# Performance work log

Measured on AMD Instinct MI355X. Metric: run time of the kernel, lower is better.

Reference implementation:

```python
import jax, jax.numpy as jnp
import numpy as np

NEG = 1e12  # matches torch code's -1e12 masking constant


def _rope_sincos(seq_len, dim, dtype):
    # SinusoidalPositionEmbedding with merge_mode='zero':
    # emb[n, i] pairs -> reshape to [n, dim] as [sin0, cos0, sin1, cos1, ...]
    pos = jnp.arange(seq_len, dtype=jnp.float32)
    inv = jnp.power(10000.0, -2.0 * jnp.arange(dim // 2, dtype=jnp.float32) / dim)
    ang = pos[:, None] * inv[None, :]            # [n, d/2]
    sin, cos = jnp.sin(ang), jnp.cos(ang)
    # cos_pos = pos[..., 1::2].repeat_interleave(2) == repeat(cos, 2)
    cos_pos = jnp.repeat(cos, 2, axis=-1).astype(dtype)  # [n, d]
    sin_pos = jnp.repeat(sin, 2, axis=-1).astype(dtype)  # [n, d]
    return sin_pos, cos_pos


def _rotate_half(x):
    # stack([-x[..., 1::2], x[..., ::2]], -1).reshape(x.shape)
    x2 = jnp.stack([-x[..., 1::2], x[..., ::2]], axis=-1)
    return x2.reshape(x.shape)


def setup_inputs() -> dict:
    key = jax.random.key(0)
    k1, k2, k3 = jax.random.split(key, 3)
    B, N, H = 8, 1024, 768
    heads, head_size = 12, 64
    inputs = jax.random.normal(k1, (B, N, H), dtype=jnp.float32)
    mask = jnp.ones((B, N), dtype=jnp.float32)
    W = jax.random.normal(k2, (H, heads * head_size * 2), dtype=jnp.float32) * (H ** -0.5)
    b = jnp.zeros((heads * head_size * 2,), dtype=jnp.float32)
    return {"inputs": inputs, "mask": mask, "W": W, "b": b}


def reference(inputs, mask, W, b):
    heads, head_size = 12, 64
    B, N, _ = inputs.shape
    x = inputs @ W + b                              # [B, N, heads*head_size*2]
    x = x.reshape(B, N, heads, 2 * head_size)       # split+stack over heads
    qw, kw = x[..., :head_size], x[..., head_size:]  # [B, N, heads, d]

    sin_pos, cos_pos = _rope_sincos(N, head_size, inputs.dtype)
    sin_pos = sin_pos[None, :, None, :]             # [1, N, 1, d]
    cos_pos = cos_pos[None, :, None, :]
    qw = qw * cos_pos + _rotate_half(qw) * sin_pos
    kw = kw * cos_pos + _rotate_half(kw) * sin_pos

    logits = jnp.einsum('bmhd,bnhd->bhmn', qw, kw)  # [B, heads, N, N]

    m1 = mask[:, None, :, None]                     # mask rows (axis ndim-2)
    m2 = mask[:, None, None, :]                     # mask cols (axis ndim-1)
    logits = logits * m1 + (-NEG) * (1.0 - m1)
    logits = logits * m2 + (-NEG) * (1.0 - m2)
    tril = jnp.tril(jnp.ones((N, N), dtype=logits.dtype), k=-1)
    logits = logits - tril * NEG                    # forbid end < start
    return logits / (head_size ** 0.5)
```

## Files before the change

kernel.cpp:

```cpp
#include <hip/hip_runtime.h>
#include <stdint.h>

#define NEGC 1000000000000.0f

using f32x4  = __attribute__((ext_vector_type(4))) float;
using short8 = __attribute__((ext_vector_type(8))) short;

typedef __attribute__((address_space(3))) uint32_t* lds_ptr_t;
typedef const __attribute__((address_space(1))) uint32_t* gptr_t;

__device__ __forceinline__ void gload_lds16(const void* g, const void* l) {
  __builtin_amdgcn_global_load_lds((gptr_t)g, (lds_ptr_t)l, 16, 0, 0);
}

__device__ __forceinline__ unsigned short f2bf(float f) {
  union { float f; uint32_t u; } v; v.f = f;
  uint32_t u = v.u;
  return (unsigned short)((u + 0x7fffu + ((u >> 16) & 1u)) >> 16);
}

__global__ __launch_bounds__(256) void k_prep(
    const float* __restrict__ in, unsigned short* __restrict__ inb,
    const float* __restrict__ W, unsigned short* __restrict__ Wt,
    float* __restrict__ ssin, float* __restrict__ scos) {
  __shared__ float tile[64][65];
  const int bx = blockIdx.x, t = threadIdx.x;
  if (bx < 6144) {
    int idx = bx * 256 + t;
    float4 v = ((const float4*)in)[idx];
    ushort4 o;
    o.x = f2bf(v.x); o.y = f2bf(v.y); o.z = f2bf(v.z); o.w = f2bf(v.w);
    ((ushort4*)inb)[idx] = o;
  } else if (bx < 6432) {
    int b = bx - 6144;
    int kb = b % 12, nb = b / 12;
    int c = t & 63, r0 = t >> 6;
#pragma unroll
    for (int p = 0; p < 16; ++p) {
      int r = r0 + p * 4;
      tile[r][c] = W[(size_t)(kb * 64 + r) * 1536 + nb * 64 + c];
    }
    __syncthreads();
#pragma unroll
    for (int p = 0; p < 16; ++p) {
      int n = r0 + p * 4;
      Wt[(size_t)(nb * 64 + n) * 768 + kb * 64 + c] = f2bf(tile[c][n]);
    }
  } else {
    int idx = (bx - 6432) * 256 + t;
    int m = idx >> 5, i = idx & 31;
    float inv = expf(-(float)i * (9.210340371976184f / 32.0f));
    float ang = (float)m * inv;
    ssin[idx] = sinf(ang);
    scos[idx] = cosf(ang);
  }
}

__global__ __launch_bounds__(256) void k_gemm1(
    const unsigned short* __restrict__ A,
    const unsigned short* __restrict__ Bt,
    const float* __restrict__ bias,
    const float* __restrict__ ssin, const float* __restrict__ scos,
    unsigned short* __restrict__ qb, unsigned short* __restrict__ kb) {
  __shared__ __align__(16) unsigned short As[2][128 * 64];
  __shared__ __align__(16) unsigned short Bs[2][128 * 64];
  const int tid = threadIdx.x;
  const int wave = tid >> 6, lane = tid & 63;
  const int wm = wave >> 1, wn = wave & 1;
  const int orig = blockIdx.x;
  const int xcd = orig & 7, idx = orig >> 3;
  const int mt8 = idx / 12;
  const int h   = idx - mt8 * 12;
  const int m0  = (xcd * 8 + mt8) * 128;
  const int j0  = h * 128;
  const int lr = lane >> 3, kc = lane & 7;

  f32x4 acc[4][4] = {};

#define STAGE1(buf, kt)                                                              \
  {                                                                                  \
    const int k0_ = (kt) * 64;                                                       \
    _Pragma("unroll")                                                                \
    for (int i = 0; i < 4; ++i) {                                                    \
      int row = i * 32 + wave * 8 + lr;                                              \
      int gk = k0_ + ((kc ^ (row & 7)) << 3);                                        \
      gload_lds16(&A[(size_t)(m0 + row) * 768 + gk], &As[buf][(i * 32 + wave * 8) * 64]); \
    }                                                                                \
    _Pragma("unroll")                                                                \
    for (int i = 0; i < 4; ++i) {                                                    \
      int row = i * 32 + wave * 8 + lr;                                              \
      int gk = k0_ + ((kc ^ (row & 7)) << 3);                                        \
      gload_lds16(&Bt[(size_t)(j0 + row) * 768 + gk], &Bs[buf][(i * 32 + wave * 8) * 64]); \
    }                                                                                \
  }

  STAGE1(0, 0);
  asm volatile("s_waitcnt vmcnt(0)" ::: "memory");
  __syncthreads();

  int cur = 0;
  for (int kt = 0; kt < 12; ++kt) {
    if (kt < 11) STAGE1(cur ^ 1, kt + 1);
#pragma unroll
    for (int kh = 0; kh < 2; ++kh) {
      short8 af[4], bfr[4];
#pragma unroll
      for (int mt = 0; mt < 4; ++mt) {
        int row = wm * 64 + mt * 16 + (lane & 15);
        int cs = (kh * 4 + (lane >> 4)) ^ (row & 7);
        af[mt] = *(const short8*)&As[cur][row * 64 + cs * 8];
      }
#pragma unroll
      for (int nt = 0; nt < 4; ++nt) {
        int row = wn * 64 + nt * 16 + (lane & 15);
        int cs = (kh * 4 + (lane >> 4)) ^ (row & 7);
        bfr[nt] = *(const short8*)&Bs[cur][row * 64 + cs * 8];
      }
#pragma unroll
      for (int mt = 0; mt < 4; ++mt)
#pragma unroll
        for (int nt = 0; nt < 4; ++nt)
          acc[mt][nt] = __builtin_amdgcn_mfma_f32_16x16x32_bf16(af[mt], bfr[nt], acc[mt][nt], 0, 0, 0);
    }
    if (kt < 11) {
      asm volatile("s_waitcnt vmcnt(0)" ::: "memory");
      __syncthreads();
      cur ^= 1;
    }
  }
#undef STAGE1

  const int col = lane & 15, rquad = lane >> 4;
  unsigned short* dst = (wn == 0) ? qb : kb;
#pragma unroll
  for (int nt = 0; nt < 4; ++nt) {
    const int d = nt * 16 + col;
    const float bv = bias[j0 + wn * 64 + d];
    const int ifr = d >> 1;
    const float sgn = (d & 1) ? 1.0f : -1.0f;
#pragma unroll
    for (int mt = 0; mt < 4; ++mt) {
#pragma unroll
      for (int j = 0; j < 4; ++j) {
        int mg = m0 + wm * 64 + mt * 16 + rquad * 4 + j;
        int ms = mg & 1023, bi = mg >> 10;
        float v = acc[mt][nt][j] + bv;
        float p = __shfl_xor(v, 1, 64);
        float s = ssin[ms * 32 + ifr], cv = scos[ms * 32 + ifr];
        float r = v * cv + sgn * p * s;
        dst[(size_t)((bi * 12 + h) * 1024 + ms) * 64 + d] = f2bf(r);
      }
    }
  }
}

__global__ __launch_bounds__(256) void k_gemm2(
    const unsigned short* __restrict__ qb, const unsigned short* __restrict__ kbuf,
    const float* __restrict__ mask, float* __restrict__ out) {
  __shared__ __align__(16) unsigned short Qs[128 * 64];
  __shared__ __align__(16) unsigned short Ks[128 * 64];
  const int tid = threadIdx.x;
  const int wave = tid >> 6, lane = tid & 63;
  const int wm = wave >> 1, wn = wave & 1;
  const int orig = blockIdx.x;
  const int xcd = orig & 7, idx = orig >> 3;
  const int bh = xcd * 12 + (idx >> 6);
  const int tt = idx & 63;
  const int tm = tt >> 3, tn = tt & 7;
  const int b = bh / 12;
  const int lr = lane >> 3, kc = lane & 7;

  const unsigned short* qbase = qb   + (size_t)bh * (1024 * 64);
  const unsigned short* kbase = kbuf + (size_t)bh * (1024 * 64);

#pragma unroll
  for (int i = 0; i < 4; ++i) {
    int row = i * 32 + wave * 8 + lr;
    int gk = (kc ^ (row & 7)) << 3;
    gload_lds16(&qbase[(size_t)(tm * 128 + row) * 64 + gk], &Qs[(i * 32 + wave * 8) * 64]);
  }
#pragma unroll
  for (int i = 0; i < 4; ++i) {
    int row = i * 32 + wave * 8 + lr;
    int gk = (kc ^ (row & 7)) << 3;
    gload_lds16(&kbase[(size_t)(tn * 128 + row) * 64 + gk], &Ks[(i * 32 + wave * 8) * 64]);
  }
  asm volatile("s_waitcnt vmcnt(0)" ::: "memory");
  __syncthreads();

  f32x4 acc[4][4] = {};
#pragma unroll
  for (int kh = 0; kh < 2; ++kh) {
    short8 af[4], bfr[4];
#pragma unroll
    for (int mt = 0; mt < 4; ++mt) {
      int row = wm * 64 + mt * 16 + (lane & 15);
      int cs = (kh * 4 + (lane >> 4)) ^ (row & 7);
      af[mt] = *(const short8*)&Qs[row * 64 + cs * 8];
    }
#pragma unroll
    for (int nt = 0; nt < 4; ++nt) {
      int row = wn * 64 + nt * 16 + (lane & 15);
      int cs = (kh * 4 + (lane >> 4)) ^ (row & 7);
      bfr[nt] = *(const short8*)&Ks[row * 64 + cs * 8];
    }
#pragma unroll
    for (int mt = 0; mt < 4; ++mt)
#pragma unroll
      for (int nt = 0; nt < 4; ++nt)
        acc[mt][nt] = __builtin_amdgcn_mfma_f32_16x16x32_bf16(af[mt], bfr[nt], acc[mt][nt], 0, 0, 0);
  }

  float* obase = out + (size_t)bh * (1024 * 1024);
  const int col = lane & 15, rquad = lane >> 4;
  float m2v[4]; int ngv[4];
#pragma unroll
  for (int nt = 0; nt < 4; ++nt) {
    ngv[nt] = tn * 128 + wn * 64 + nt * 16 + col;
    m2v[nt] = mask[b * 1024 + ngv[nt]];
  }
#pragma unroll
  for (int mt = 0; mt < 4; ++mt) {
#pragma unroll
    for (int j = 0; j < 4; ++j) {
      int mg = tm * 128 + wm * 64 + mt * 16 + rquad * 4 + j;
      float m1 = mask[b * 1024 + mg];
      float* orow = obase + (size_t)mg * 1024;
#pragma unroll
      for (int nt = 0; nt < 4; ++nt) {
        float v = acc[mt][nt][j];
        v = v * m1 - NEGC * (1.0f - m1);
        v = v * m2v[nt] - NEGC * (1.0f - m2v[nt]);
        if (ngv[nt] < mg) v -= NEGC;
        orow[ngv[nt]] = v * 0.125f;
      }
    }
  }
}

extern "C" void kernel_launch(void* const* d_in, const int* in_sizes, int n_in,
                              void* d_out, int out_size, void* d_ws, size_t ws_size,
                              hipStream_t stream) {
  const float* inputs = (const float*)d_in[0];
  const float* mask   = (const float*)d_in[1];
  const float* W      = (const float*)d_in[2];
  const float* bias   = (const float*)d_in[3];
  float* out = (float*)d_out;
  char* ws = (char*)d_ws;

  float* ssin = (float*)(ws);
  float* scos = (float*)(ws + 131072);
  unsigned short* inA = (unsigned short*)(ws + 262144);
  unsigned short* Wt  = (unsigned short*)(ws + 262144 + 12582912);
  unsigned short* qb  = (unsigned short*)(ws + 262144 + 12582912 + 2359296);
  unsigned short* kb  = (unsigned short*)(ws + 262144 + 12582912 + 2359296 + 12582912);

  hipLaunchKernelGGL(k_prep, dim3(6560), dim3(256), 0, stream,
                     inputs, inA, W, Wt, ssin, scos);
  hipLaunchKernelGGL(k_gemm1, dim3(768), dim3(256), 0, stream,
                     inA, Wt, bias, ssin, scos, qb, kb);
  hipLaunchKernelGGL(k_gemm2, dim3(6144), dim3(256), 0, stream, qb, kb, mask, out);
}
```

Before: 130.9 us.

## Make QK^T blocks loop over key tiles with double-buffered K prefetch

The logits kernel now gives each block one 128-row Q tile, loaded into LDS once. The block walks all 8 key tiles in sequence, and the next K tile is fetched into a second LDS buffer while the current one is computed and stored. Row masks are loaded once per block, and the grid drops from 6144 to 768 blocks. The aim is to cut redundant Q loads and per-block launch overhead, and to hide K load latency behind the large output stores. The risks are lower parallelism, since only three blocks exist per CU, and a wait of vmcnt(63) that may not actually ensure the prefetched K data has landed before the barrier.

```diff
diff --git a/kernel.cpp b/kernel.cpp
--- a/kernel.cpp
+++ b/kernel.cpp
@@ -158,20 +158,31 @@
     const unsigned short* __restrict__ qb, const unsigned short* __restrict__ kbuf,
     const float* __restrict__ mask, float* __restrict__ out) {
   __shared__ __align__(16) unsigned short Qs[128 * 64];
-  __shared__ __align__(16) unsigned short Ks[128 * 64];
+  __shared__ __align__(16) unsigned short Ks[2][128 * 64];
   const int tid = threadIdx.x;
   const int wave = tid >> 6, lane = tid & 63;
   const int wm = wave >> 1, wn = wave & 1;
   const int orig = blockIdx.x;
   const int xcd = orig & 7, idx = orig >> 3;
-  const int bh = xcd * 12 + (idx >> 6);
-  const int tt = idx & 63;
-  const int tm = tt >> 3, tn = tt & 7;
+  const int bh = xcd * 12 + (idx >> 3);
+  const int tm = idx & 7;
   const int b = bh / 12;
   const int lr = lane >> 3, kc = lane & 7;
 
   const unsigned short* qbase = qb   + (size_t)bh * (1024 * 64);
   const unsigned short* kbase = kbuf + (size_t)bh * (1024 * 64);
+  float* obase = out + (size_t)bh * (1024 * 1024);
+
+#define STAGEK(buf, tn_)                                                             \
+  {                                                                                  \
+    _Pragma("unroll")                                                                \
+    for (int i = 0; i < 4; ++i) {                                                    \
+      int row = i * 32 + wave * 8 + lr;                                              \
+      int gk = (kc ^ (row & 7)) << 3;                                                \
+      gload_lds16(&kbase[(size_t)((tn_) * 128 + row) * 64 + gk],                     \
+                  &Ks[buf][(i * 32 + wave * 8) * 64]);                               \
+    }                                                                                \
+  }
 
 #pragma unroll
   for (int i = 0; i < 4; ++i) {
@@ -179,63 +190,78 @@
     int gk = (kc ^ (row & 7)) << 3;
     gload_lds16(&qbase[(size_t)(tm * 128 + row) * 64 + gk], &Qs[(i * 32 + wave * 8) * 64]);
   }
-#pragma unroll
-  for (int i = 0; i < 4; ++i) {
-    int row = i * 32 + wave * 8 + lr;
-    int gk = (kc ^ (row & 7)) << 3;
-    gload_lds16(&kbase[(size_t)(tn * 128 + row) * 64 + gk], &Ks[(i * 32 + wave * 8) * 64]);
-  }
+  STAGEK(0, 0);
   asm volatile("s_waitcnt vmcnt(0)" ::: "memory");
   __syncthreads();
 
-  f32x4 acc[4][4] = {};
-#pragma unroll
-  for (int kh = 0; kh < 2; ++kh) {
-    short8 af[4], bfr[4];
-#pragma unroll
-    for (int mt = 0; mt < 4; ++mt) {
-      int row = wm * 64 + mt * 16 + (lane & 15);
-      int cs = (kh * 4 + (lane >> 4)) ^ (row & 7);
-      af[mt] = *(const short8*)&Qs[row * 64 + cs * 8];
-    }
-#pragma unroll
-    for (int nt = 0; nt < 4; ++nt) {
-      int row = wn * 64 + nt * 16 + (lane & 15);
-      int cs = (kh * 4 + (lane >> 4)) ^ (row & 7);
-      bfr[nt] = *(const short8*)&Ks[row * 64 + cs * 8];
-    }
-#pragma unroll
-    for (int mt = 0; mt < 4; ++mt)
-#pragma unroll
-      for (int nt = 0; nt < 4; ++nt)
-        acc[mt][nt] = __builtin_amdgcn_mfma_f32_16x16x32_bf16(af[mt], bfr[nt], acc[mt][nt], 0, 0, 0);
-  }
-
-  float* obase = out + (size_t)bh * (1024 * 1024);
   const int col = lane & 15, rquad = lane >> 4;
-  float m2v[4]; int ngv[4];
-#pragma unroll
-  for (int nt = 0; nt < 4; ++nt) {
-    ngv[nt] = tn * 128 + wn * 64 + nt * 16 + col;
-    m2v[nt] = mask[b * 1024 + ngv[nt]];
-  }
-#pragma unroll
-  for (int mt = 0; mt < 4; ++mt) {
+  float m1v[4][4];
+#pragma unroll
+  for (int mt = 0; mt < 4; ++mt)
 #pragma unroll
     for (int j = 0; j < 4; ++j) {
       int mg = tm * 128 + wm * 64 + mt * 16 + rquad * 4 + j;
-      float m1 = mask[b * 1024 + mg];
-      float* orow = obase + (size_t)mg * 1024;
+      m1v[mt][j] = mask[b * 1024 + mg];
+    }
+
+  int cur = 0;
+  for (int t = 0; t < 8; ++t) {
+    if (t < 7) STAGEK(cur ^ 1, t + 1);
+
+    f32x4 acc[4][4] = {};
+#pragma unroll
+    for (int kh = 0; kh < 2; ++kh) {
+      short8 af[4], bfr[4];
+#pragma unroll
+      for (int mt = 0; mt < 4; ++mt) {
+        int row = wm * 64 + mt * 16 + (lane & 15);
+        int cs = (kh * 4 + (lane >> 4)) ^ (row & 7);
+        af[mt] = *(const short8*)&Qs[row * 64 + cs * 8];
+      }
 #pragma unroll
       for (int nt = 0; nt < 4; ++nt) {
-        float v = acc[mt][nt][j];
-        v = v * m1 - NEGC * (1.0f - m1);
-        v = v * m2v[nt] - NEGC * (1.0f - m2v[nt]);
-        if (ngv[nt] < mg) v -= NEGC;
-        orow[ngv[nt]] = v * 0.125f;
-      }
-    }
-  }
+        int row = wn * 64 + nt * 16 + (lane & 15);
+        int cs = (kh * 4 + (lane >> 4)) ^ (row & 7);
+        bfr[nt] = *(const short8*)&Ks[cur][row * 64 + cs * 8];
+      }
+#pragma unroll
+      for (int mt = 0; mt < 4; ++mt)
+#pragma unroll
+        for (int nt = 0; nt < 4; ++nt)
+          acc[mt][nt] = __builtin_amdgcn_mfma_f32_16x16x32_bf16(af[mt], bfr[nt], acc[mt][nt], 0, 0, 0);
+    }
+
+    float m2v[4]; int ngv[4];
+#pragma unroll
+    for (int nt = 0; nt < 4; ++nt) {
+      ngv[nt] = t * 128 + wn * 64 + nt * 16 + col;
+      m2v[nt] = mask[b * 1024 + ngv[nt]];
+    }
+#pragma unroll
+    for (int mt = 0; mt < 4; ++mt) {
+#pragma unroll
+      for (int j = 0; j < 4; ++j) {
+        int mg = tm * 128 + wm * 64 + mt * 16 + rquad * 4 + j;
+        float m1 = m1v[mt][j];
+        float* orow = obase + (size_t)mg * 1024;
+#pragma unroll
+        for (int nt = 0; nt < 4; ++nt) {
+          float v = acc[mt][nt][j];
+          v = v * m1 - NEGC * (1.0f - m1);
+          v = v * m2v[nt] - NEGC * (1.0f - m2v[nt]);
+          if (ngv[nt] < mg) v -= NEGC;
+          orow[ngv[nt]] = v * 0.125f;
+        }
+      }
+    }
+
+    if (t < 7) {
+      asm volatile("s_waitcnt vmcnt(63)" ::: "memory");
+      asm volatile("s_barrier" ::: "memory");
+      cur ^= 1;
+    }
+  }
+#undef STAGEK
 }
 
 extern "C" void kernel_launch(void* const* d_in, const int* in_sizes, int n_in,
@@ -259,5 +285,5 @@
                      inputs, inA, W, Wt, ssin, scos);
   hipLaunchKernelGGL(k_gemm1, dim3(768), dim3(256), 0, stream,
                      inA, Wt, bias, ssin, scos, qb, kb);
-  hipLaunchKernelGGL(k_gemm2, dim3(6144), dim3(256), 0, stream, qb, kb, mask, out);
-}
+  hipLaunchKernelGGL(k_gemm2, dim3(768), dim3(256), 0, stream, qb, kb, mask, out);
+}
```

New measurement: 136.9 us. 1.05x slower.
